# Kernel tuning notes

Measured on AMD Instinct MI355X. Metric: run time of the kernel, lower is better.

The kernel has to match this reference:

```python
import jax, jax.numpy as jnp
import numpy as np

FT = 0.2  # clip floor (init arg ft)

def _norm_mat(m):
    # matrix / (count of nonzeros along last dim + 1e-30)
    deg = jnp.sum(m != 0, axis=-1, keepdims=True).astype(m.dtype)
    return m / (deg + 1e-30)

def _l2n(x):
    return x / (jnp.linalg.norm(x, axis=-1, keepdims=True) + 1e-30)

def setup_inputs():
    B, L, D, H, O = 2, 2048, 64, 64, 128
    N = 2 * L
    ks = jax.random.split(jax.random.key(0), 30)
    u = lambda i, s: jax.random.uniform(ks[i], s, jnp.float32)
    g = lambda i, s: jax.random.normal(ks[i], s, jnp.float32) * 0.05
    inp = {}
    inp['word_outputs_0'] = g(0, (B, L, D))
    inp['word_outputs_1'] = g(1, (B, L, D))
    inp['node_hidden'] = g(2, (B, D))
    inp['op_embedding'] = g(3, (B, O, D))
    inp['word_exist_sequence'] = (u(4, (B, N)) < 0.8).astype(jnp.float32)
    inp['word_exist_matrix'] = (u(5, (B, N, N)) < 0.8).astype(jnp.float32)
    inp['word_operator'] = (u(6, (B, N, O)) < 0.02).astype(jnp.float32)
    inp['word_word'] = (u(7, (B, N, N)) < 0.01).astype(jnp.float32)
    inp['depend_0'] = (u(8, (B, L, L)) < 0.05).astype(jnp.float32)
    inp['depend_1'] = (u(9, (B, L, L)) < 0.05).astype(jnp.float32)
    inp['goal_word'] = u(10, (B, N))
    names = [('Wg', (D, H)), ('bg', (H,)), ('Wwk', (D, H)), ('bwk', (H,)),
             ('Wws', (D, H)), ('bws', (H,)), ('Wo', (D, D)), ('bo', (D,)),
             ('Wupd', (3 * H, D)), ('bupd', (D,)), ('Wf', (3 * H + D, D)), ('bf', (D,)),
             ('Wf2', (2 * D, D)), ('bf2', (D,)), ('Wout', (D, D)), ('bout', (D,))]
    for i, (nm, s) in enumerate(names):
        inp[nm] = g(11 + i, s)
    return inp

def _forward(w0, w1, nh, opE, wes, wem, wop, ww, d0, d1, gw,
             Wg, bg, Wwk, bwk, Wws, bws, Wo, bo, Wupd, bupd, Wf, bf, Wf2, bf2, Wout, bout):
    all_w = jnp.concatenate([w0, w1], axis=1)                      # [B,N,D]
    goal_trans = (nh @ Wg + bg)[:, None, :]                        # [B,1,H] (broadcast = expand)
    word_g = _l2n(goal_trans * gw[..., None])                      # [B,N,H]
    word_w_k = _l2n(jnp.matmul(_norm_mat(ww * wem), all_w @ Wwk + bwk))
    ws0 = jnp.matmul(_norm_mat(d0), w0 @ Wws + bws)
    ws1 = jnp.matmul(_norm_mat(d1), w1 @ Wws + bws)
    word_w_s = _l2n(jnp.concatenate([ws0, ws1], axis=1))           # [B,N,H]
    neigh = jnp.concatenate([word_g, word_w_k, word_w_s], axis=-1)  # [B,N,3H]
    forget = jax.nn.sigmoid(jnp.concatenate([all_w, word_g, word_w_k, word_w_s], axis=-1) @ Wf + bf)
    word_updated = jnp.maximum(forget, FT) * all_w + (1.0 - forget) * jax.nn.relu(neigh @ Wupd + bupd)
    adj_op = _norm_mat(jnp.swapaxes(wes[..., None] * wop, 1, 2))   # [B,O,N]
    word_op = jnp.matmul(adj_op, word_updated @ Wo + bo)           # [B,O,D]
    forget2 = jax.nn.sigmoid(jnp.concatenate([opE, word_op], axis=-1) @ Wf2 + bf2)
    op_out = jnp.maximum(forget2, FT) * opE + (1.0 - forget2) * jax.nn.relu(word_op @ Wout + bout)
    # original returns (split(word_updated), op_embedding); concat along node axis here
    return jnp.concatenate([word_updated, op_out], axis=1)         # [B,N+O,D]

def reference(word_outputs_0, word_outputs_1, node_hidden, op_embedding,
              word_exist_sequence, word_exist_matrix, word_operator, word_word,
              depend_0, depend_1, goal_word,
              Wg, bg, Wwk, bwk, Wws, bws, Wo, bo, Wupd, bupd, Wf, bf, Wf2, bf2, Wout, bout):
    return _forward(word_outputs_0, word_outputs_1, node_hidden, op_embedding,
                    word_exist_sequence, word_exist_matrix, word_operator, word_word,
                    depend_0, depend_1, goal_word,
                    Wg, bg, Wwk, bwk, Wws, bws, Wo, bo, Wupd, bupd, Wf, bf, Wf2, bf2, Wout, bout)
```

## Files before the change

kernel.cpp:

```cpp
#include <hip/hip_runtime.h>
#include <cstdint>

typedef unsigned short u16;
typedef unsigned long long u64;

__device__ __forceinline__ u16 f2b(float f){
  union { float f; uint32_t i; } v; v.f = f;
  uint32_t r = v.i + 0x7FFFu + ((v.i >> 16) & 1u);
  return (u16)(r >> 16);
}
__device__ __forceinline__ float b2f(u16 u){
  union { uint32_t i; float f; } v; v.i = ((uint32_t)u) << 16; return v.f;
}
__device__ __forceinline__ float sigmoidf(float x){ return 1.0f / (1.0f + __expf(-x)); }

__global__ __launch_bounds__(256) void k_prep(
    const float* __restrict__ w0, const float* __restrict__ w1,
    uint32_t* __restrict__ wpk){
  int tid = threadIdx.x, blk = blockIdx.x;
  int b = blk >> 6;
  int j = (blk & 63) * 64 + (tid >> 2);
  int part = tid & 3;
  const float* src = (j < 2048) ? (w0 + ((size_t)(b*2048 + j))*64 + part*16)
                                : (w1 + ((size_t)(b*2048 + j - 2048))*64 + part*16);
  uint32_t* dst = wpk + ((size_t)b*4096 + j)*32 + part*8;
  float4 v0 = ((const float4*)src)[0];
  float4 v1 = ((const float4*)src)[1];
  float4 v2 = ((const float4*)src)[2];
  float4 v3 = ((const float4*)src)[3];
  uint4 o0, o1;
  o0.x = (uint32_t)f2b(v0.x) | ((uint32_t)f2b(v0.y) << 16);
  o0.y = (uint32_t)f2b(v0.z) | ((uint32_t)f2b(v0.w) << 16);
  o0.z = (uint32_t)f2b(v1.x) | ((uint32_t)f2b(v1.y) << 16);
  o0.w = (uint32_t)f2b(v1.z) | ((uint32_t)f2b(v1.w) << 16);
  o1.x = (uint32_t)f2b(v2.x) | ((uint32_t)f2b(v2.y) << 16);
  o1.y = (uint32_t)f2b(v2.z) | ((uint32_t)f2b(v2.w) << 16);
  o1.z = (uint32_t)f2b(v3.x) | ((uint32_t)f2b(v3.y) << 16);
  o1.w = (uint32_t)f2b(v3.z) | ((uint32_t)f2b(v3.w) << 16);
  ((uint4*)dst)[0] = o0;
  ((uint4*)dst)[1] = o1;
}

__global__ __launch_bounds__(256) void k_bits(
    const float* __restrict__ ww, const float* __restrict__ wem,
    const float* __restrict__ d0, const float* __restrict__ d1,
    const float* __restrict__ wes, const float* __restrict__ wop,
    const uint32_t* __restrict__ wpk,
    const float* __restrict__ nh, const float* __restrict__ Wg, const float* __restrict__ bg,
    const float* __restrict__ Wf, const float* __restrict__ Wupd, const float* __restrict__ Wo,
    u16* __restrict__ psumB, int* __restrict__ pcntB,
    u16* __restrict__ psumD, int* __restrict__ pcntD,
    u64* __restrict__ bitOp, float* __restrict__ ghat,
    uint32_t* __restrict__ pkWf, uint32_t* __restrict__ pkWu, uint32_t* __restrict__ pkWo){
  __shared__ int q[4][288];
  int tid = threadIdx.x, wave = tid >> 6, lane = tid & 63;
  int bid = blockIdx.x;
  if (bid >= 2048){
    if (bid >= 2304){
      int aux = bid - 2304;
      if (aux == 16){
        if (tid < 128){
          int b = tid >> 6, h = tid & 63;
          float g = bg[h];
          for (int d = 0; d < 64; ++d) g += nh[b*64 + d] * Wg[d*64 + h];
          float ss = g * g;
          #pragma unroll
          for (int o = 32; o > 0; o >>= 1) ss += __shfl_xor(ss, o, 64);
          ghat[b*64 + h] = g / (sqrtf(ss) + 1e-30f);
        }
        return;
      }
      for (int k = tid; k < 1024; k += 256){
        int i = aux*1024 + k;
        const float* src; uint32_t* dst; int li;
        if (i < 8192){ src = Wf; dst = pkWf; li = i; }
        else if (i < 14336){ src = Wupd; dst = pkWu; li = i - 8192; }
        else { src = Wo; dst = pkWo; li = i - 14336; }
        int k2 = li >> 6, ln = li & 63;
        dst[li] = (uint32_t)f2b(src[(2*k2)*64 + ln]) | ((uint32_t)f2b(src[(2*k2+1)*64 + ln]) << 16);
      }
      return;
    }
    int w = (bid - 2048)*4 + wave;
    int ng0 = w * 8;
    #pragma unroll
    for (int i = 0; i < 8; ++i){
      int n = ng0 + i;
      float vx = wop[(size_t)n*128 + lane];
      float vy = wop[(size_t)n*128 + 64 + lane];
      float e  = wes[n];
      u64 m0 = __ballot((e != 0.f) && (vx != 0.f));
      u64 m1 = __ballot((e != 0.f) && (vy != 0.f));
      if (lane == 0) bitOp[(size_t)n*2]     = m0;
      if (lane == 1) bitOp[(size_t)n*2 + 1] = m1;
    }
    return;
  }
  int wid = bid*4 + wave;
  float4 a0, a1, a2, a3;
#define ISSUE_MASKS(tt) { \
  int t_ = (tt); \
  const float* A_; \
  if (t_ < 32768){ \
    int row_ = t_ >> 2, ch_ = t_ & 3; \
    A_ = ww + (size_t)row_*4096 + ch_*1024; \
  } else { \
    int idx_ = t_ - 32768, rowp_ = idx_ >> 1, ch_ = idx_ & 1; \
    if (rowp_ < 4096) A_ = d0 + (size_t)rowp_*2048 + ch_*1024; \
    else { int rr_ = rowp_ - 4096; A_ = d1 + (size_t)rr_*2048 + ch_*1024; } \
  } \
  const float4* ra_ = (const float4*)A_ + lane; \
  a0 = ra_[0]; a1 = ra_[64]; a2 = ra_[128]; a3 = ra_[192]; }
  ISSUE_MASKS(wid)
  int half = lane >> 5;
  int dcol = lane & 31;
  #pragma unroll 1
  for (int it = 0; it < 6; ++it){
    int t = wid + it*8192;
    bool big = (t < 32768);
    const uint32_t* wub;
    const float* wemRow;
    u16* ps; int* pc;
    if (big){
      int row = t >> 2, chunk = t & 3;
      int b = row >> 12;
      wub = wpk + (size_t)b*131072 + (size_t)(chunk*1024)*32 + dcol;
      wemRow = wem + (size_t)row*4096 + chunk*1024;
      ps = psumB + (size_t)t*64; pc = pcntB + t;
    } else {
      int idx = t - 32768, rowp = idx >> 1, chunk = idx & 1;
      int b, jadd = chunk*1024;
      if (rowp < 4096){ b = rowp >> 11; }
      else { int rr = rowp - 4096; b = rr >> 11; jadd += 2048; }
      wub = wpk + (size_t)b*131072 + (size_t)jadd*32 + dcol;
      wemRow = wem;
      ps = psumD + (size_t)idx*64; pc = pcntD + idx;
    }
    u64 myw = 0;
#define B4(i, va) { \
  u64 m0 = __ballot(va.x != 0.f); \
  u64 m1 = __ballot(va.y != 0.f); \
  u64 m2 = __ballot(va.z != 0.f); \
  u64 m3 = __ballot(va.w != 0.f); \
  if (lane == (i)*4 + 0) myw = m0; \
  if (lane == (i)*4 + 1) myw = m1; \
  if (lane == (i)*4 + 2) myw = m2; \
  if (lane == (i)*4 + 3) myw = m3; }
    B4(0, a0) B4(1, a1) B4(2, a2) B4(3, a3)
#undef B4
    int c = __popcll(myw);
    int pre = c;
    #pragma unroll
    for (int off = 1; off < 64; off <<= 1){
      int tt = __shfl_up(pre, off, 64);
      if (lane >= off) pre += tt;
    }
    int total = __shfl(pre, 63, 64);
    int base = pre - c;
    int colhi = (lane >> 2) * 256 + (lane & 3);
    u64 m = myw;
    while (m){
      int p = __builtin_ctzll(m); m &= m - 1;
      q[wave][base++] = colhi + p*4;
    }
    int totP = (total + 31) & ~31;
    if (lane < totP - total) q[wave][total + lane] = 0;
    if (it < 5) ISSUE_MASKS(t + 8192)
    float accE = 0.f, accO = 0.f;
    int nb = totP >> 5;
    uint32_t g0[16], g1[16];
    if (big){
      float m0a[16], m1a[16];
      int vc = 0;
#define GISSB(arr, wma, bi) { int bse = (bi) << 5; \
  _Pragma("unroll") for (int k2 = 0; k2 < 16; ++k2){ \
    int j = q[wave][bse + 2*k2 + half]; \
    arr[k2] = wub[(size_t)j*32]; \
    wma[k2] = wemRow[j]; } }
#define GACCB(arr, wma, bi) { int bse = (bi) << 5; \
  _Pragma("unroll") for (int k2 = 0; k2 < 16; ++k2){ \
    bool v = ((bse + 2*k2 + half) < total) && (wma[k2] != 0.f); \
    uint32_t wv = arr[k2]; \
    accE += v ? b2f((u16)wv) : 0.f; \
    accO += v ? b2f((u16)(wv >> 16)) : 0.f; \
    vc += v ? 1 : 0; } }
      if (nb > 0) GISSB(g0, m0a, 0)
      for (int bi = 0; bi < nb; bi += 2){
        if (bi + 1 < nb) GISSB(g1, m1a, bi + 1)
        GACCB(g0, m0a, bi)
        if (bi + 1 < nb){
          if (bi + 2 < nb) GISSB(g0, m0a, bi + 2)
          GACCB(g1, m1a, bi + 1)
        }
      }
#undef GISSB
#undef GACCB
      accE += __shfl_xor(accE, 32, 64);
      accO += __shfl_xor(accO, 32, 64);
      vc   += __shfl_xor(vc, 32, 64);
      if (lane < 32)
        ((uint32_t*)ps)[lane] = (uint32_t)f2b(accE) | ((uint32_t)f2b(accO) << 16);
      if (lane == 0) pc[0] = vc;
    } else {
#define GISS(arr, bi) { int bse = (bi) << 5; \
  _Pragma("unroll") for (int k2 = 0; k2 < 16; ++k2){ \
    int j = q[wave][bse + 2*k2 + half]; \
    arr[k2] = wub[(size_t)j*32]; } }
#define GACC(arr, bi) { int bse = (bi) << 5; \
  _Pragma("unroll") for (int k2 = 0; k2 < 16; ++k2){ \
    bool v = (bse + 2*k2 + half) < total; \
    uint32_t wv = arr[k2]; \
    accE += v ? b2f((u16)wv) : 0.f; \
    accO += v ? b2f((u16)(wv >> 16)) : 0.f; } }
      if (nb > 0) GISS(g0, 0)
      for (int bi = 0; bi < nb; bi += 2){
        if (bi + 1 < nb) GISS(g1, bi + 1)
        GACC(g0, bi)
        if (bi + 1 < nb){
          if (bi + 2 < nb) GISS(g0, bi + 2)
          GACC(g1, bi + 1)
        }
      }
#undef GISS
#undef GACC
      accE += __shfl_xor(accE, 32, 64);
      accO += __shfl_xor(accO, 32, 64);
      if (lane < 32)
        ((uint32_t*)ps)[lane] = (uint32_t)f2b(accE) | ((uint32_t)f2b(accO) << 16);
      if (lane == 0) pc[0] = total;
    }
  }
#undef ISSUE_MASKS
}

__global__ __launch_bounds__(256, 2) void k_mid(
    const u16* __restrict__ psumB, const int* __restrict__ pcntB,
    const u16* __restrict__ psumD, const int* __restrict__ pcntD,
    const float* __restrict__ Wwk, const float* __restrict__ bwk,
    const float* __restrict__ Wws, const float* __restrict__ bws,
    const float* __restrict__ w0, const float* __restrict__ w1,
    const float* __restrict__ gw, const float* __restrict__ ghat,
    const uint32_t* __restrict__ pkWf, const uint32_t* __restrict__ pkWu,
    const uint32_t* __restrict__ pkWo,
    const float* __restrict__ bf, const float* __restrict__ bupd, const float* __restrict__ bo,
    float* __restrict__ out, float* __restrict__ WUo){
  __shared__ uint32_t ldsU[16384];
  __shared__ float xsh[4][256];
  int tid = threadIdx.x, lane = tid & 63, wave = tid >> 6;
  float* sWk = (float*)ldsU;
  float* sWs = (float*)ldsU + 4096;
  for (int i = tid; i < 1024; i += 256){
    ((float4*)sWk)[i] = ((const float4*)Wwk)[i];
    ((float4*)sWs)[i] = ((const float4*)Wws)[i];
  }
  __syncthreads();
  float bwkL = bwk[lane], bwsL = bws[lane];
  float wk[4], wsv[4], aw[4], wgv[4];
  #pragma unroll
  for (int t = 0; t < 4; ++t){
    int row = blockIdx.x*4 + wave + t*2048;
    int b = row >> 12, n = row & 4095;
    float S = b2f(psumB[((size_t)row*4 + 0)*64 + lane]) + b2f(psumB[((size_t)row*4 + 1)*64 + lane])
            + b2f(psumB[((size_t)row*4 + 2)*64 + lane]) + b2f(psumB[((size_t)row*4 + 3)*64 + lane]);
    int T = pcntB[row*4] + pcntB[row*4 + 1] + pcntB[row*4 + 2] + pcntB[row*4 + 3];
    float y = (float)T * bwkL;
    #pragma unroll 8
    for (int d = 0; d < 64; ++d) y += __shfl(S, d, 64) * sWk[d*64 + lane];
    float ss = y * y;
    #pragma unroll
    for (int o = 32; o > 0; o >>= 1) ss += __shfl_xor(ss, o, 64);
    wk[t] = y / (sqrtf(ss) + 1e-30f);
    int rp = (n < 2048) ? (b*2048 + n) : (4096 + b*2048 + (n - 2048));
    float S2 = b2f(psumD[((size_t)rp*2 + 0)*64 + lane]) + b2f(psumD[((size_t)rp*2 + 1)*64 + lane]);
    int T2 = pcntD[rp*2] + pcntD[rp*2 + 1];
    float y2 = (float)T2 * bwsL;
    #pragma unroll 8
    for (int d = 0; d < 64; ++d) y2 += __shfl(S2, d, 64) * sWs[d*64 + lane];
    float ss2 = y2 * y2;
    #pragma unroll
    for (int o = 32; o > 0; o >>= 1) ss2 += __shfl_xor(ss2, o, 64);
    wsv[t] = y2 / (sqrtf(ss2) + 1e-30f);
    aw[t] = (n < 2048) ? w0[((size_t)(b*2048 + n))*64 + lane]
                       : w1[((size_t)(b*2048 + n - 2048))*64 + lane];
    wgv[t] = (gw[b*4096 + n] != 0.f) ? ghat[b*64 + lane] : 0.f;
  }
  __syncthreads();
  uint32_t* pWf = ldsU;
  uint32_t* pWu = ldsU + 8192;
  uint32_t* pWo = ldsU + 14336;
  for (int i = tid; i < 2048; i += 256) ((uint4*)pWf)[i] = ((const uint4*)pkWf)[i];
  for (int i = tid; i < 1536; i += 256) ((uint4*)pWu)[i] = ((const uint4*)pkWu)[i];
  for (int i = tid; i < 512;  i += 256) ((uint4*)pWo)[i] = ((const uint4*)pkWo)[i];
  __syncthreads();
  float bff = bf[lane], bup = bupd[lane], boo = bo[lane];
  #pragma unroll
  for (int t = 0; t < 4; ++t){
    int row = blockIdx.x*4 + wave + t*2048;
    int b = row >> 12, n = row & 4095;
    xsh[wave][lane] = aw[t]; xsh[wave][64 + lane] = wgv[t];
    xsh[wave][128 + lane] = wk[t]; xsh[wave][192 + lane] = wsv[t];
    float f = bff, u = bup;
    #pragma unroll 8
    for (int k2 = 0; k2 < 32; ++k2){
      float2 xv = *(const float2*)&xsh[wave][2*k2];
      uint32_t wf = pWf[k2*64 + lane];
      f += xv.x * b2f((u16)wf) + xv.y * b2f((u16)(wf >> 16));
    }
    #pragma unroll 8
    for (int k2 = 32; k2 < 128; ++k2){
      float2 xv = *(const float2*)&xsh[wave][2*k2];
      uint32_t wf = pWf[k2*64 + lane];
      uint32_t wu = pWu[(k2 - 32)*64 + lane];
      f += xv.x * b2f((u16)wf) + xv.y * b2f((u16)(wf >> 16));
      u += xv.x * b2f((u16)wu) + xv.y * b2f((u16)(wu >> 16));
    }
    f = sigmoidf(f);
    u = fmaxf(u, 0.f);
    float wu = fmaxf(f, 0.2f) * aw[t] + (1.f - f) * u;
    out[((size_t)b*4224 + n)*64 + lane] = wu;
    float o = boo;
    #pragma unroll 8
    for (int k2 = 0; k2 < 32; ++k2){
      uint32_t wo2 = pWo[k2*64 + lane];
      o += __shfl(wu, 2*k2, 64) * b2f((u16)wo2) + __shfl(wu, 2*k2 + 1, 64) * b2f((u16)(wo2 >> 16));
    }
    WUo[(size_t)row*64 + lane] = o;
  }
}

__global__ __launch_bounds__(256) void k_opfin(
    const u64* __restrict__ bitOp, const float* __restrict__ WUo,
    const float* __restrict__ opE,
    const float* __restrict__ Wf2, const float* __restrict__ bf2,
    const float* __restrict__ Wout, const float* __restrict__ bout,
    float* __restrict__ out){
  __shared__ float sW2[8192];
  __shared__ float sWo[4096];
  __shared__ int q[4][96];
  __shared__ float sacc[4][64];
  __shared__ int scnt[4];
  __shared__ float xsh[128];
  int tid = threadIdx.x, lane = tid & 63, wave = tid >> 6;
  for (int i = tid; i < 2048; i += 256) ((float4*)sW2)[i] = ((const float4*)Wf2)[i];
  for (int i = tid; i < 1024; i += 256) ((float4*)sWo)[i] = ((const float4*)Wout)[i];
  int rowIdx = blockIdx.x;
  int b = rowIdx >> 7, o = rowIdx & 127;
  int wrd = o >> 6, bit = o & 63;
  const u64* bp = bitOp + (size_t)b*8192 + (size_t)wave*2048 + wrd;
  u64 lt = (1ULL << lane) - 1ULL;
  u64 vv[16];
  #pragma unroll
  for (int it = 0; it < 16; ++it) vv[it] = bp[(size_t)(it*64 + lane)*2];
  int cnt = 0;
  #pragma unroll
  for (int it = 0; it < 16; ++it){
    bool nz = (vv[it] >> bit) & 1ULL;
    u64 m = __ballot(nz);
    if (nz) q[wave][cnt + (int)__popcll(m & lt)] = wave*1024 + it*64 + lane;
    cnt += (int)__popcll(m);
  }
  const float* Xb = WUo + (size_t)b*4096*64 + lane;
  float acc = 0.f;
  int i = 0;
  for (; i + 8 <= cnt; i += 8){
    int4 c0 = *(const int4*)&q[wave][i];
    int4 c1 = *(const int4*)&q[wave][i + 4];
    float v0 = Xb[(size_t)c0.x*64], v1 = Xb[(size_t)c0.y*64];
    float v2 = Xb[(size_t)c0.z*64], v3 = Xb[(size_t)c0.w*64];
    float v4 = Xb[(size_t)c1.x*64], v5 = Xb[(size_t)c1.y*64];
    float v6 = Xb[(size_t)c1.z*64], v7 = Xb[(size_t)c1.w*64];
    acc += ((v0 + v1) + (v2 + v3)) + ((v4 + v5) + (v6 + v7));
  }
  for (; i < cnt; ++i) acc += Xb[(size_t)q[wave][i]*64];
  sacc[wave][lane] = acc;
  if (lane == 0) scnt[wave] = cnt;
  __syncthreads();
  if (wave == 0){
    float t = sacc[0][lane] + sacc[1][lane] + sacc[2][lane] + sacc[3][lane];
    float deg = (float)(scnt[0] + scnt[1] + scnt[2] + scnt[3]);
    float wo = t / (deg + 1e-30f);
    float e  = opE[(size_t)rowIdx*64 + lane];
    xsh[lane] = e; xsh[64 + lane] = wo;
    float f = bf2[lane], u = bout[lane];
    #pragma unroll 8
    for (int k = 0; k < 128; ++k) f += xsh[k] * sW2[k*64 + lane];
    #pragma unroll 8
    for (int d = 0; d < 64; ++d)  u += xsh[64 + d] * sWo[d*64 + lane];
    f = sigmoidf(f);
    u = fmaxf(u, 0.f);
    float res = fmaxf(f, 0.2f) * e + (1.f - f) * u;
    out[((size_t)b*4224 + 4096 + o)*64 + lane] = res;
  }
}

extern "C" void kernel_launch(void* const* d_in, const int* in_sizes, int n_in,
                              void* d_out, int out_size, void* d_ws, size_t ws_size,
                              hipStream_t stream){
  const float* w0   = (const float*)d_in[0];
  const float* w1   = (const float*)d_in[1];
  const float* nh   = (const float*)d_in[2];
  const float* opE  = (const float*)d_in[3];
  const float* wes  = (const float*)d_in[4];
  const float* wem  = (const float*)d_in[5];
  const float* wop  = (const float*)d_in[6];
  const float* ww   = (const float*)d_in[7];
  const float* d0   = (const float*)d_in[8];
  const float* d1   = (const float*)d_in[9];
  const float* gw   = (const float*)d_in[10];
  const float* Wg   = (const float*)d_in[11];
  const float* bg   = (const float*)d_in[12];
  const float* Wwk  = (const float*)d_in[13];
  const float* bwk  = (const float*)d_in[14];
  const float* Wws  = (const float*)d_in[15];
  const float* bws  = (const float*)d_in[16];
  const float* Wo   = (const float*)d_in[17];
  const float* bo   = (const float*)d_in[18];
  const float* Wupd = (const float*)d_in[19];
  const float* bupd = (const float*)d_in[20];
  const float* Wf   = (const float*)d_in[21];
  const float* bf   = (const float*)d_in[22];
  const float* Wf2  = (const float*)d_in[23];
  const float* bf2  = (const float*)d_in[24];
  const float* Wout = (const float*)d_in[25];
  const float* bout = (const float*)d_in[26];

  float* ws    = (float*)d_ws;
  float* ghat  = ws;
  uint32_t* pkWf = (uint32_t*)(ws + 128);
  uint32_t* pkWu = (uint32_t*)(ws + 8320);
  uint32_t* pkWo = (uint32_t*)(ws + 14464);
  u64*  bitOp  = (u64*)(ws + 16512);
  u16*  psumB  = (u16*)(ws + 49280);
  int*  pcntB  = (int*)(ws + 1097856);
  u16*  psumD  = (u16*)(ws + 1130624);
  int*  pcntD  = (int*)(ws + 1654912);
  float* WUo   = ws + 2195584;
  uint32_t* wpk = (uint32_t*)(ws + 2719872);
  float* out   = (float*)d_out;

  k_prep<<<128, 256, 0, stream>>>(w0, w1, wpk);
  k_bits<<<2321, 256, 0, stream>>>(ww, wem, d0, d1, wes, wop, wpk,
                                   nh, Wg, bg, Wf, Wupd, Wo,
                                   psumB, pcntB, psumD, pcntD,
                                   bitOp, ghat, pkWf, pkWu, pkWo);
  k_mid<<<512, 256, 0, stream>>>(psumB, pcntB, psumD, pcntD,
                                 Wwk, bwk, Wws, bws, w0, w1, gw, ghat,
                                 pkWf, pkWu, pkWo, bf, bupd, bo, out, WUo);
  k_opfin<<<256, 256, 0, stream>>>(bitOp, WUo, opE, Wf2, bf2, Wout, bout, out);
}
```

Before: 411.4 us.

## Assign one full row per wave in k_bits instead of chunked partial sums

The k_bits sparse-gather kernel now processes a whole 4096-wide word_word row and a whole 2048-wide dependency row per wave, rather than splitting rows into 1024-column chunks across six loop iterations. Partial sums and counts are written once per row, so k_mid no longer reads and adds four or two bf16 partials, and the workspace shrinks. The valid-count test is replaced with a multiply by the mask value. This cuts partial-sum traffic and bf16 rounding steps, but it lowers per-wave parallel granularity and loses the cross-iteration prefetch of the next mask chunk, so load balance and latency hiding may change.

New measurement: 410.9 us (median of 2 runs). Within noise of the previous version (-0.1%).

```diff
diff --git a/kernel.cpp b/kernel.cpp
--- a/kernel.cpp
+++ b/kernel.cpp
@@ -97,81 +97,59 @@
     return;
   }
   int wid = bid*4 + wave;
-  float4 a0, a1, a2, a3;
-#define ISSUE_MASKS(tt) { \
-  int t_ = (tt); \
-  const float* A_; \
-  if (t_ < 32768){ \
-    int row_ = t_ >> 2, ch_ = t_ & 3; \
-    A_ = ww + (size_t)row_*4096 + ch_*1024; \
-  } else { \
-    int idx_ = t_ - 32768, rowp_ = idx_ >> 1, ch_ = idx_ & 1; \
-    if (rowp_ < 4096) A_ = d0 + (size_t)rowp_*2048 + ch_*1024; \
-    else { int rr_ = rowp_ - 4096; A_ = d1 + (size_t)rr_*2048 + ch_*1024; } \
-  } \
-  const float4* ra_ = (const float4*)A_ + lane; \
-  a0 = ra_[0]; a1 = ra_[64]; a2 = ra_[128]; a3 = ra_[192]; }
-  ISSUE_MASKS(wid)
-  int half = lane >> 5;
-  int dcol = lane & 31;
-  #pragma unroll 1
-  for (int it = 0; it < 6; ++it){
-    int t = wid + it*8192;
-    bool big = (t < 32768);
-    const uint32_t* wub;
-    const float* wemRow;
-    u16* ps; int* pc;
-    if (big){
-      int row = t >> 2, chunk = t & 3;
-      int b = row >> 12;
-      wub = wpk + (size_t)b*131072 + (size_t)(chunk*1024)*32 + dcol;
-      wemRow = wem + (size_t)row*4096 + chunk*1024;
-      ps = psumB + (size_t)t*64; pc = pcntB + t;
-    } else {
-      int idx = t - 32768, rowp = idx >> 1, chunk = idx & 1;
-      int b, jadd = chunk*1024;
-      if (rowp < 4096){ b = rowp >> 11; }
-      else { int rr = rowp - 4096; b = rr >> 11; jadd += 2048; }
-      wub = wpk + (size_t)b*131072 + (size_t)jadd*32 + dcol;
-      wemRow = wem;
-      ps = psumD + (size_t)idx*64; pc = pcntD + idx;
-    }
-    u64 myw = 0;
-#define B4(i, va) { \
-  u64 m0 = __ballot(va.x != 0.f); \
-  u64 m1 = __ballot(va.y != 0.f); \
-  u64 m2 = __ballot(va.z != 0.f); \
-  u64 m3 = __ballot(va.w != 0.f); \
-  if (lane == (i)*4 + 0) myw = m0; \
-  if (lane == (i)*4 + 1) myw = m1; \
-  if (lane == (i)*4 + 2) myw = m2; \
-  if (lane == (i)*4 + 3) myw = m3; }
-    B4(0, a0) B4(1, a1) B4(2, a2) B4(3, a3)
-#undef B4
-    int c = __popcll(myw);
-    int pre = c;
+  int half = lane >> 5, dcol = lane & 31;
+  int colhi = (lane >> 2) * 256 + (lane & 3);
+  float4 a[8];
+  u64 myw = 0;
+  const float4* r0 = (const float4*)(ww + (size_t)wid*4096) + lane;
+  #pragma unroll
+  for (int i = 0; i < 8; ++i) a[i] = r0[i*64];
+#define BAL8(wb) { \
+  _Pragma("unroll") for (int i = 0; i < 8; ++i){ \
+    u64 m0 = __ballot(a[i].x != 0.f); \
+    u64 m1 = __ballot(a[i].y != 0.f); \
+    u64 m2 = __ballot(a[i].z != 0.f); \
+    u64 m3 = __ballot(a[i].w != 0.f); \
+    if (lane == (wb) + i*4 + 0) myw = m0; \
+    if (lane == (wb) + i*4 + 1) myw = m1; \
+    if (lane == (wb) + i*4 + 2) myw = m2; \
+    if (lane == (wb) + i*4 + 3) myw = m3; } }
+  BAL8(0)
+  #pragma unroll
+  for (int i = 0; i < 8; ++i) a[i] = r0[512 + i*64];
+  BAL8(32)
+  int c = __popcll(myw);
+  int pre = c;
+  #pragma unroll
+  for (int off = 1; off < 64; off <<= 1){
+    int tt = __shfl_up(pre, off, 64);
+    if (lane >= off) pre += tt;
+  }
+  int total = __shfl(pre, 63, 64);
+  int base = pre - c;
+  u64 m = myw;
+  while (m){
+    int p = __builtin_ctzll(m); m &= m - 1;
+    q[wave][base++] = colhi + p*4;
+  }
+  int totP = (total + 31) & ~31;
+  if (lane < totP - total) q[wave][total + lane] = 0;
+  const float* depBase; int jadd, bdep;
+  if (wid < 4096){ depBase = d0 + (size_t)wid*2048; jadd = 0; bdep = wid >> 11; }
+  else { int rr = wid - 4096; depBase = d1 + (size_t)rr*2048; jadd = 2048; bdep = rr >> 11; }
+  {
+    const float4* r2 = (const float4*)depBase + lane;
     #pragma unroll
-    for (int off = 1; off < 64; off <<= 1){
-      int tt = __shfl_up(pre, off, 64);
-      if (lane >= off) pre += tt;
-    }
-    int total = __shfl(pre, 63, 64);
-    int base = pre - c;
-    int colhi = (lane >> 2) * 256 + (lane & 3);
-    u64 m = myw;
-    while (m){
-      int p = __builtin_ctzll(m); m &= m - 1;
-      q[wave][base++] = colhi + p*4;
-    }
-    int totP = (total + 31) & ~31;
-    if (lane < totP - total) q[wave][total + lane] = 0;
-    if (it < 5) ISSUE_MASKS(t + 8192)
-    float accE = 0.f, accO = 0.f;
+    for (int i = 0; i < 8; ++i) a[i] = r2[i*64];
+  }
+  {
+    int b = wid >> 12;
+    const uint32_t* wub = wpk + (size_t)b*131072 + dcol;
+    const float* wemRow = wem + (size_t)wid*4096;
+    float accE = 0.f, accO = 0.f, vcF = 0.f;
     int nb = totP >> 5;
     uint32_t g0[16], g1[16];
-    if (big){
-      float m0a[16], m1a[16];
-      int vc = 0;
+    float m0a[16], m1a[16];
 #define GISSB(arr, wma, bi) { int bse = (bi) << 5; \
   _Pragma("unroll") for (int k2 = 0; k2 < 16; ++k2){ \
     int j = q[wave][bse + 2*k2 + half]; \
@@ -179,29 +157,54 @@
     wma[k2] = wemRow[j]; } }
 #define GACCB(arr, wma, bi) { int bse = (bi) << 5; \
   _Pragma("unroll") for (int k2 = 0; k2 < 16; ++k2){ \
-    bool v = ((bse + 2*k2 + half) < total) && (wma[k2] != 0.f); \
+    float sel = ((bse + 2*k2 + half) < total) ? wma[k2] : 0.f; \
     uint32_t wv = arr[k2]; \
-    accE += v ? b2f((u16)wv) : 0.f; \
-    accO += v ? b2f((u16)(wv >> 16)) : 0.f; \
-    vc += v ? 1 : 0; } }
-      if (nb > 0) GISSB(g0, m0a, 0)
-      for (int bi = 0; bi < nb; bi += 2){
-        if (bi + 1 < nb) GISSB(g1, m1a, bi + 1)
-        GACCB(g0, m0a, bi)
-        if (bi + 1 < nb){
-          if (bi + 2 < nb) GISSB(g0, m0a, bi + 2)
-          GACCB(g1, m1a, bi + 1)
-        }
+    accE += sel * b2f((u16)wv); \
+    accO += sel * b2f((u16)(wv >> 16)); \
+    vcF += sel; } }
+    if (nb > 0) GISSB(g0, m0a, 0)
+    for (int bi = 0; bi < nb; bi += 2){
+      if (bi + 1 < nb) GISSB(g1, m1a, bi + 1)
+      GACCB(g0, m0a, bi)
+      if (bi + 1 < nb){
+        if (bi + 2 < nb) GISSB(g0, m0a, bi + 2)
+        GACCB(g1, m1a, bi + 1)
       }
+    }
 #undef GISSB
 #undef GACCB
-      accE += __shfl_xor(accE, 32, 64);
-      accO += __shfl_xor(accO, 32, 64);
-      vc   += __shfl_xor(vc, 32, 64);
-      if (lane < 32)
-        ((uint32_t*)ps)[lane] = (uint32_t)f2b(accE) | ((uint32_t)f2b(accO) << 16);
-      if (lane == 0) pc[0] = vc;
-    } else {
+    accE += __shfl_xor(accE, 32, 64);
+    accO += __shfl_xor(accO, 32, 64);
+    vcF  += __shfl_xor(vcF, 32, 64);
+    if (lane < 32)
+      ((uint32_t*)(psumB + (size_t)wid*64))[lane] =
+        (uint32_t)f2b(accE) | ((uint32_t)f2b(accO) << 16);
+    if (lane == 0) pcntB[wid] = (int)(vcF + 0.5f);
+  }
+  myw = 0;
+  BAL8(0)
+#undef BAL8
+  c = __popcll(myw);
+  pre = c;
+  #pragma unroll
+  for (int off = 1; off < 64; off <<= 1){
+    int tt = __shfl_up(pre, off, 64);
+    if (lane >= off) pre += tt;
+  }
+  total = __shfl(pre, 63, 64);
+  base = pre - c;
+  m = myw;
+  while (m){
+    int p = __builtin_ctzll(m); m &= m - 1;
+    q[wave][base++] = colhi + p*4;
+  }
+  totP = (total + 31) & ~31;
+  if (lane < totP - total) q[wave][total + lane] = 0;
+  {
+    const uint32_t* wub = wpk + (size_t)bdep*131072 + (size_t)jadd*32 + dcol;
+    float accE = 0.f, accO = 0.f;
+    int nb = totP >> 5;
+    uint32_t g0[16], g1[16];
 #define GISS(arr, bi) { int bse = (bi) << 5; \
   _Pragma("unroll") for (int k2 = 0; k2 < 16; ++k2){ \
     int j = q[wave][bse + 2*k2 + half]; \
@@ -212,25 +215,24 @@
     uint32_t wv = arr[k2]; \
     accE += v ? b2f((u16)wv) : 0.f; \
     accO += v ? b2f((u16)(wv >> 16)) : 0.f; } }
-      if (nb > 0) GISS(g0, 0)
-      for (int bi = 0; bi < nb; bi += 2){
-        if (bi + 1 < nb) GISS(g1, bi + 1)
-        GACC(g0, bi)
-        if (bi + 1 < nb){
-          if (bi + 2 < nb) GISS(g0, bi + 2)
-          GACC(g1, bi + 1)
-        }
+    if (nb > 0) GISS(g0, 0)
+    for (int bi = 0; bi < nb; bi += 2){
+      if (bi + 1 < nb) GISS(g1, bi + 1)
+      GACC(g0, bi)
+      if (bi + 1 < nb){
+        if (bi + 2 < nb) GISS(g0, bi + 2)
+        GACC(g1, bi + 1)
       }
+    }
 #undef GISS
 #undef GACC
-      accE += __shfl_xor(accE, 32, 64);
-      accO += __shfl_xor(accO, 32, 64);
-      if (lane < 32)
-        ((uint32_t*)ps)[lane] = (uint32_t)f2b(accE) | ((uint32_t)f2b(accO) << 16);
-      if (lane == 0) pc[0] = total;
-    }
-  }
-#undef ISSUE_MASKS
+    accE += __shfl_xor(accE, 32, 64);
+    accO += __shfl_xor(accO, 32, 64);
+    if (lane < 32)
+      ((uint32_t*)(psumD + (size_t)wid*64))[lane] =
+        (uint32_t)f2b(accE) | ((uint32_t)f2b(accO) << 16);
+    if (lane == 0) pcntD[wid] = total;
+  }
 }
 
 __global__ __launch_bounds__(256, 2) void k_mid(
@@ -260,9 +262,8 @@
   for (int t = 0; t < 4; ++t){
     int row = blockIdx.x*4 + wave + t*2048;
     int b = row >> 12, n = row & 4095;
-    float S = b2f(psumB[((size_t)row*4 + 0)*64 + lane]) + b2f(psumB[((size_t)row*4 + 1)*64 + lane])
-            + b2f(psumB[((size_t)row*4 + 2)*64 + lane]) + b2f(psumB[((size_t)row*4 + 3)*64 + lane]);
-    int T = pcntB[row*4] + pcntB[row*4 + 1] + pcntB[row*4 + 2] + pcntB[row*4 + 3];
+    float S = b2f(psumB[(size_t)row*64 + lane]);
+    int T = pcntB[row];
     float y = (float)T * bwkL;
     #pragma unroll 8
     for (int d = 0; d < 64; ++d) y += __shfl(S, d, 64) * sWk[d*64 + lane];
@@ -271,8 +272,8 @@
     for (int o = 32; o > 0; o >>= 1) ss += __shfl_xor(ss, o, 64);
     wk[t] = y / (sqrtf(ss) + 1e-30f);
     int rp = (n < 2048) ? (b*2048 + n) : (4096 + b*2048 + (n - 2048));
-    float S2 = b2f(psumD[((size_t)rp*2 + 0)*64 + lane]) + b2f(psumD[((size_t)rp*2 + 1)*64 + lane]);
-    int T2 = pcntD[rp*2] + pcntD[rp*2 + 1];
+    float S2 = b2f(psumD[(size_t)rp*64 + lane]);
+    int T2 = pcntD[rp];
     float y2 = (float)T2 * bwsL;
     #pragma unroll 8
     for (int d = 0; d < 64; ++d) y2 += __shfl(S2, d, 64) * sWs[d*64 + lane];
@@ -431,11 +432,11 @@
   uint32_t* pkWo = (uint32_t*)(ws + 14464);
   u64*  bitOp  = (u64*)(ws + 16512);
   u16*  psumB  = (u16*)(ws + 49280);
-  int*  pcntB  = (int*)(ws + 1097856);
-  u16*  psumD  = (u16*)(ws + 1130624);
-  int*  pcntD  = (int*)(ws + 1654912);
-  float* WUo   = ws + 2195584;
-  uint32_t* wpk = (uint32_t*)(ws + 2719872);
+  int*  pcntB  = (int*)(ws + 311424);
+  u16*  psumD  = (u16*)(ws + 319616);
+  int*  pcntD  = (int*)(ws + 581760);
+  float* WUo   = ws + 589952;
+  uint32_t* wpk = (uint32_t*)(ws + 1114240);
   float* out   = (float*)d_out;
 
   k_prep<<<128, 256, 0, stream>>>(w0, w1, wpk);
```
